# Kernel optimization log

Hardware: AMD Instinct MI355X
Metric: run time of the kernel (lower is better)

The kernel has to match this reference:

```python
import jax, jax.numpy as jnp
import numpy as np

N = 8192
IN = 128   # in_channels
CH = 64    # conv_ch


def setup_inputs() -> dict:
    key = jax.random.key(0)
    ks = jax.random.split(key, 8)
    p = lambda k, shape: jax.random.normal(k, shape, jnp.float32) * 0.02
    return {
        "x": jax.random.normal(ks[0], (N, IN), jnp.float32),
        "edge_index": jax.random.randint(ks[1], (N, N), 0, 2, jnp.int32),
        "W1": p(ks[2], (IN, CH)),      "b1": jnp.zeros((CH,), jnp.float32),
        "W2": p(ks[3], (CH, 2 * CH)),  "b2": jnp.zeros((2 * CH,), jnp.float32),
        "We": p(ks[4], (2 * CH, CH)),  "be": jnp.zeros((CH,), jnp.float32),
        "Wd1": p(ks[5], (2 * CH, CH)), "bd1": jnp.zeros((CH,), jnp.float32),
        "Wd2": p(ks[6], (CH, IN)),     "bd2": jnp.zeros((IN,), jnp.float32),
    }


def _norm_adj(edge_index):
    # PyG GCNConv: A_hat = A + I (self loops appended), sym norm D^-1/2 A_hat D^-1/2
    A = (edge_index != 0).astype(jnp.float32)
    A = A + jnp.eye(A.shape[0], dtype=jnp.float32)
    deg = A.sum(axis=1)
    dinv = jnp.where(deg > 0.0, jax.lax.rsqrt(deg), 0.0)
    return dinv[:, None] * A * dinv[None, :]  # [N, N]


def _gcn(nadj, x, W, b):
    return nadj @ (x @ W) + b


def _lrelu(v):
    return jax.nn.leaky_relu(v, 0.01)  # torch default negative_slope


def reference(x, edge_index, W1, b1, W2, b2, We, be, Wd1, bd1, Wd2, bd2):
    nadj = _norm_adj(edge_index)
    h = _lrelu(_gcn(nadj, x, W1, b1))          # [N, CH]
    z = _lrelu(_gcn(nadj, h, W2, b2))          # [N, 2*CH]
    re = _lrelu(_gcn(nadj, z, We, be))         # [N, CH]
    recon_edge = jax.nn.sigmoid(re @ re.T)     # [N, N]
    xd = _lrelu(_gcn(nadj, z, Wd1, bd1))       # [N, CH]
    x_out = _lrelu(_gcn(nadj, xd, Wd2, bd2))   # [N, IN]
    return (recon_edge, x_out, z)
```

## Files before the change

### kernel.cpp

```cpp
#include <hip/hip_runtime.h>
#include <hip/hip_bf16.h>
#include <stdint.h>

typedef unsigned short u16;
typedef unsigned char u8;
typedef unsigned int u32;
typedef __attribute__((ext_vector_type(8))) short frag8;
typedef __attribute__((ext_vector_type(4))) float f4;

#define N8K 8192
#define SK 4
#define NKT 256
#define NT2 128


__device__ __forceinline__ u16 f2bf(float f) {
  union { float f; unsigned u; } v; v.f = f;
  return (u16)((v.u + 0x7FFFu + ((v.u >> 16) & 1u)) >> 16);
}
__device__ __forceinline__ float lrelu(float v) { return v > 0.f ? v : 0.01f * v; }

__device__ __forceinline__ void expand4(u32 w, u32& o0, u32& o1) {
  u32 hi = __builtin_amdgcn_perm(0u, 0x00403F00u, w);
  u32 lo = __builtin_amdgcn_perm(0u, 0x00008000u, w);
  o0 = __builtin_amdgcn_perm(hi, lo, 0x05010400u);
  o1 = __builtin_amdgcn_perm(hi, lo, 0x07030602u);
}

#define WQ(col) (((col) & 31) >> 3)
#define SHIFT(col) (8 * (((col) & 7) & 3) + 2 * (((col) & 7) >> 2) + 4 * ((col) >> 5))

__global__ __launch_bounds__(256) void k_deg(const int* __restrict__ e,
                                             u8* __restrict__ at,
                                             float* __restrict__ dinv) {
  int Rt = blockIdx.x;
  int t = threadIdx.x;
  int rl = t & 15;
  int row = Rt * 16 + rl;
  int tg = t >> 4;
  int diagT2 = row >> 6;
  int cnt = 0;
  __shared__ int cs[256];
  for (int p = 0; p < 8; ++p) {
    int T2 = tg + 16 * p;
    const int4* src = (const int4*)(e + (size_t)row * N8K + T2 * 64);
    u32 w[4] = {0u, 0u, 0u, 0u};
#pragma unroll
    for (int q8 = 0; q8 < 16; ++q8) {
      int4 v = src[q8];
      u32 c0 = (v.x != 0), c1 = (v.y != 0), c2 = (v.z != 0), c3 = (v.w != 0);
      cnt += (int)(c0 + c1 + c2 + c3);
      const int cb = q8 * 4;
      w[WQ(cb + 0)] |= c0 << SHIFT(cb + 0);
      w[WQ(cb + 1)] |= c1 << SHIFT(cb + 1);
      w[WQ(cb + 2)] |= c2 << SHIFT(cb + 2);
      w[WQ(cb + 3)] |= c3 << SHIFT(cb + 3);
    }
    if (T2 == diagT2) {
      int col = row & 63;
      int qd = (col & 31) >> 3;
      u32 add = 1u << (8 * ((col & 7) & 3) + 2 * ((col & 7) >> 2) + 4 * (col >> 5));
#pragma unroll
      for (int q = 0; q < 4; ++q)
        if (q == qd) w[q] += add;
      cnt += 1;
    }
    u8* dst = at + ((size_t)(Rt * NT2 + T2) * 64 + rl) * 4;
#pragma unroll
    for (int q = 0; q < 4; ++q)
      *(u32*)(dst + (size_t)(16 * q) * 4) = w[q];
  }
  cs[t] = cnt;
  __syncthreads();
  if (t < 16) {
    int s = 0;
#pragma unroll
    for (int g = 0; g < 16; ++g) s += cs[t + 16 * g];
    dinv[Rt * 16 + t] = 1.0f / sqrtf((float)s);
  }
}

__global__ __launch_bounds__(256, 2) void k_sgemm1(const float* __restrict__ Xf,
                                                   const float* __restrict__ Wa,
                                                   const float* __restrict__ dinv,
                                                   u16* __restrict__ Pt) {
  const int KT = 4;
  __shared__ __attribute__((aligned(16))) u16 Wt[8 * 4 * 64 * 8];
  int t = threadIdx.x, mt = blockIdx.x;
  int lane = t & 63, wave = t >> 6;
  for (int u = t; u < 8 * KT * 64; u += 256) {
    int l = u & 63, T = (u >> 6) % KT, nt = (u >> 6) / KT;
    int n = nt * 16 + (l & 15);
    int k0 = T * 32 + (l >> 4) * 8;
    u16 tmp[8];
#pragma unroll
    for (int j = 0; j < 8; ++j) {
      int k = k0 + j;
      float v = (n < 64) ? Wa[k * 64 + n] : 0.f;
      tmp[j] = f2bf(v);
    }
    *(uint4*)&Wt[(size_t)u * 8] = *(const uint4*)tmp;
  }
  __syncthreads();
  int wm = (wave >> 1) * 64, wn = (wave & 1) * 64;
  int fm = lane & 15, q = lane >> 4;
  f4 acc[4][4];
#pragma unroll
  for (int m = 0; m < 4; ++m)
#pragma unroll
    for (int n = 0; n < 4; ++n) acc[m][n] = (f4){0.f, 0.f, 0.f, 0.f};
  for (int T = 0; T < KT; ++T) {
    frag8 a[4], b[4];
#pragma unroll
    for (int m = 0; m < 4; ++m) {
      int Rt = mt * 8 + (wm >> 4) + m;
      const float* px = Xf + (size_t)(Rt * 16 + fm) * 128 + T * 32 + q * 8;
      float4 v0 = *(const float4*)px, v1 = *(const float4*)(px + 4);
      u16 tmp[8] = {f2bf(v0.x), f2bf(v0.y), f2bf(v0.z), f2bf(v0.w),
                    f2bf(v1.x), f2bf(v1.y), f2bf(v1.z), f2bf(v1.w)};
      a[m] = *(const frag8*)tmp;
    }
#pragma unroll
    for (int n = 0; n < 4; ++n)
      b[n] = *(const frag8*)&Wt[((size_t)(((wn >> 4) + n) * KT + T) * 64 + lane) * 8];
#pragma unroll
    for (int m = 0; m < 4; ++m)
#pragma unroll
      for (int n = 0; n < 4; ++n)
        acc[m][n] = __builtin_amdgcn_mfma_f32_16x16x32_bf16(a[m], b[n], acc[m][n], 0, 0, 0);
  }
#pragma unroll
  for (int m = 0; m < 4; ++m) {
    int ibase = mt * 128 + wm + 16 * m + q * 4;
    float d0 = dinv[ibase], d1 = dinv[ibase + 1], d2 = dinv[ibase + 2], d3 = dinv[ibase + 3];
#pragma unroll
    for (int n = 0; n < 4; ++n) {
      u32 lo = (u32)f2bf(d0 * acc[m][n][0]) | ((u32)f2bf(d1 * acc[m][n][1]) << 16);
      u32 hi = (u32)f2bf(d2 * acc[m][n][2]) | ((u32)f2bf(d3 * acc[m][n][3]) << 16);
      u32 plo = __shfl_xor(lo, 16, 64);
      u32 phi = __shfl_xor(hi, 16, 64);
      if ((q & 1) == 0) {
        uint4 u; u.x = lo; u.y = hi; u.z = plo; u.w = phi;
        int gi = mt * 128 + wm + 16 * m + (q >> 1) * 8;
        int T2 = gi >> 5;
        int lB = fm + 16 * ((gi >> 3) & 3);
        int nt = (wn >> 4) + n;
        *(uint4*)(Pt + ((size_t)(nt * NKT + T2) * 64 + lB) * 8) = u;
      }
    }
  }
}

__global__ __launch_bounds__(256, 1) void k_bgemm(const u8* __restrict__ At,
                                                  const u16* __restrict__ Bt,
                                                  float* __restrict__ Ctmp) {
  int t = threadIdx.x;
  int mt = blockIdx.x, ks = blockIdx.y;
  int lane = t & 63, wave = t >> 6;
  int wm = (wave >> 1) * 64, wn = (wave & 1) * 64;
  f4 acc[4][4];
#pragma unroll
  for (int m = 0; m < 4; ++m)
#pragma unroll
    for (int n = 0; n < 4; ++n) acc[m][n] = (f4){0.f, 0.f, 0.f, 0.f};

  const int T20 = ks * 32;
  const u8*  Ab = At + ((size_t)((mt * 8 + (wm >> 4)) * NT2 + T20) * 64 + lane) * 4;
  const u16* Bb = Bt + ((size_t)(((wn >> 4)) * NKT + 2 * T20) * 64 + lane) * 8;

#pragma unroll 2
  for (int T2 = 0; T2 < 32; ++T2) {
    u32 w[4];
    frag8 aE[4], aO[4], bE[4], bO[4];
#pragma unroll
    for (int m = 0; m < 4; ++m)
      w[m] = *(const u32*)(Ab + (size_t)m * (NT2 * 256) + (size_t)T2 * 256);
#pragma unroll
    for (int n = 0; n < 4; ++n) {
      bE[n] = *(const frag8*)(Bb + (size_t)n * (NKT * 512) + (size_t)(2 * T2) * 512);
      bO[n] = *(const frag8*)(Bb + (size_t)n * (NKT * 512) + (size_t)(2 * T2) * 512 + 512);
    }
#pragma unroll
    for (int m = 0; m < 4; ++m) {
      u32 e0 = w[m] & 0x03030303u;
      u32 e1 = (w[m] >> 2) & 0x03030303u;
      u32 e2 = (w[m] >> 4) & 0x03030303u;
      u32 e3 = (w[m] >> 6) & 0x03030303u;
      uint4 rE, rO;
      expand4(e0, rE.x, rE.y); expand4(e1, rE.z, rE.w);
      expand4(e2, rO.x, rO.y); expand4(e3, rO.z, rO.w);
      aE[m] = *(const frag8*)&rE;
      aO[m] = *(const frag8*)&rO;
    }
#pragma unroll
    for (int m = 0; m < 4; ++m)
#pragma unroll
      for (int n = 0; n < 4; ++n)
        acc[m][n] = __builtin_amdgcn_mfma_f32_16x16x32_bf16(aE[m], bE[n], acc[m][n], 0, 0, 0);
#pragma unroll
    for (int m = 0; m < 4; ++m)
#pragma unroll
      for (int n = 0; n < 4; ++n)
        acc[m][n] = __builtin_amdgcn_mfma_f32_16x16x32_bf16(aO[m], bO[n], acc[m][n], 0, 0, 0);
  }

  float* Co = Ctmp + (size_t)ks * (N8K * 128);
  int fm = lane & 15, rbase = (lane >> 4) * 4;
#pragma unroll
  for (int m = 0; m < 4; ++m) {
    int i0 = mt * 128 + wm + 16 * m + rbase;
#pragma unroll
    for (int n = 0; n < 4; ++n) {
      int c = wn + 16 * n + fm;
#pragma unroll
      for (int r = 0; r < 4; ++r) Co[(size_t)(i0 + r) * 128 + c] = acc[m][n][r];
    }
  }
}

__global__ __launch_bounds__(256, 2) void k_fuse(const float* __restrict__ Ctmp,
                                                 const float* __restrict__ dinv,
                                                 const float* __restrict__ bE,
                                                 const float* __restrict__ bE2,
                                                 float* __restrict__ outZ,
                                                 u16* __restrict__ retG,
                                                 int mode,
                                                 const float* __restrict__ Wa, int wacols,
                                                 const float* __restrict__ Wb,
                                                 u16* __restrict__ Pt) {
  __shared__ __attribute__((aligned(16))) u16 Xs[8 * 4 * 64 * 8];
  __shared__ __attribute__((aligned(16))) u16 Wt[8 * 4 * 64 * 8];
  int t = threadIdx.x, mt = blockIdx.x;
  int lane = t & 63, wave = t >> 6;
  const int KT = (mode == 2) ? 4 : 2;

  int C8 = (mode == 1) ? 8 : 16;
  int totalU = 128 * C8;
  for (int u0 = t; u0 < totalU; u0 += 256) {
    int i = (mode == 1) ? (u0 >> 3) : (u0 >> 4);
    int c8 = (mode == 1) ? (u0 & 7) : (u0 & 15);
    int gi = mt * 128 + i;
    int c0 = c8 * 8;
    float v[8];
#pragma unroll
    for (int j = 0; j < 8; ++j) v[j] = 0.f;
#pragma unroll
    for (int k = 0; k < SK; ++k) {
      const float4* p = (const float4*)(Ctmp + (size_t)k * (N8K * 128) + (size_t)gi * 128 + c0);
      float4 x0 = p[0], x1 = p[1];
      v[0] += x0.x; v[1] += x0.y; v[2] += x0.z; v[3] += x0.w;
      v[4] += x1.x; v[5] += x1.y; v[6] += x1.z; v[7] += x1.w;
    }
    float di = dinv[gi];
    u16 ob[8];
    if (mode == 3 && c8 < 8) {
#pragma unroll
      for (int j = 0; j < 8; ++j) ob[j] = f2bf(lrelu(di * v[j] + bE[c0 + j]));
      int T = c8 >> 2, l = (i & 15) + 16 * (c8 & 3);
      *(uint4*)(retG + ((size_t)((gi >> 4) * 2 + T) * 64 + l) * 8) = *(const uint4*)ob;
    } else if (mode == 3) {
      int cl = c0 - 64;
#pragma unroll
      for (int j = 0; j < 8; ++j) ob[j] = f2bf(lrelu(di * v[j] + bE2[cl + j]));
      int cp = c8 - 8;
      int T = cp >> 2, l = (i & 15) + 16 * (cp & 3);
      *(uint4*)&Xs[(((i >> 4) * 2 + T) * 64 + l) * 8] = *(const uint4*)ob;
    } else {
#pragma unroll
      for (int j = 0; j < 8; ++j) v[j] = lrelu(di * v[j] + bE[c0 + j]);
#pragma unroll
      for (int j = 0; j < 8; ++j) ob[j] = f2bf(v[j]);
      int T = c8 >> 2, l = (i & 15) + 16 * (c8 & 3);
      *(uint4*)&Xs[(((i >> 4) * KT + T) * 64 + l) * 8] = *(const uint4*)ob;
      if (mode == 2) {
        float4* po = (float4*)(outZ + (size_t)gi * 128 + c0);
        po[0] = (float4){v[0], v[1], v[2], v[3]};
        po[1] = (float4){v[4], v[5], v[6], v[7]};
      }
    }
  }

  for (int u = t; u < 8 * KT * 64; u += 256) {
    int l = u & 63, T = (u >> 6) % KT, nt = (u >> 6) / KT;
    int n = nt * 16 + (l & 15);
    int k0 = T * 32 + (l >> 4) * 8;
    u16 tmp[8];
#pragma unroll
    for (int j = 0; j < 8; ++j) {
      int k = k0 + j;
      float v = (n < wacols) ? Wa[k * wacols + n] : (Wb ? Wb[k * 64 + (n - 64)] : 0.f);
      tmp[j] = f2bf(v);
    }
    *(uint4*)&Wt[(size_t)u * 8] = *(const uint4*)tmp;
  }
  __syncthreads();

  int wm = (wave >> 1) * 64, wn = (wave & 1) * 64;
  int fm = lane & 15, q = lane >> 4;
  f4 acc[4][4];
#pragma unroll
  for (int m = 0; m < 4; ++m)
#pragma unroll
    for (int n = 0; n < 4; ++n) acc[m][n] = (f4){0.f, 0.f, 0.f, 0.f};
  for (int T = 0; T < KT; ++T) {
    frag8 a[4], b[4];
#pragma unroll
    for (int m = 0; m < 4; ++m)
      a[m] = *(const frag8*)&Xs[((size_t)(((wm >> 4) + m) * KT + T) * 64 + lane) * 8];
#pragma unroll
    for (int n = 0; n < 4; ++n)
      b[n] = *(const frag8*)&Wt[((size_t)(((wn >> 4) + n) * KT + T) * 64 + lane) * 8];
#pragma unroll
    for (int m = 0; m < 4; ++m)
#pragma unroll
      for (int n = 0; n < 4; ++n)
        acc[m][n] = __builtin_amdgcn_mfma_f32_16x16x32_bf16(a[m], b[n], acc[m][n], 0, 0, 0);
  }
#pragma unroll
  for (int m = 0; m < 4; ++m) {
    int ibase = mt * 128 + wm + 16 * m + q * 4;
    float d0 = dinv[ibase], d1 = dinv[ibase + 1], d2 = dinv[ibase + 2], d3 = dinv[ibase + 3];
#pragma unroll
    for (int n = 0; n < 4; ++n) {
      u32 lo = (u32)f2bf(d0 * acc[m][n][0]) | ((u32)f2bf(d1 * acc[m][n][1]) << 16);
      u32 hi = (u32)f2bf(d2 * acc[m][n][2]) | ((u32)f2bf(d3 * acc[m][n][3]) << 16);
      u32 plo = __shfl_xor(lo, 16, 64);
      u32 phi = __shfl_xor(hi, 16, 64);
      if ((q & 1) == 0) {
        uint4 u; u.x = lo; u.y = hi; u.z = plo; u.w = phi;
        int gi = mt * 128 + wm + 16 * m + (q >> 1) * 8;
        int T2 = gi >> 5;
        int lB = fm + 16 * ((gi >> 3) & 3);
        int nt = (wn >> 4) + n;
        *(uint4*)(Pt + ((size_t)(nt * NKT + T2) * 64 + lB) * 8) = u;
      }
    }
  }
}

__global__ __launch_bounds__(256) void k_epi4(const float* __restrict__ Ctmp,
                                              const float* __restrict__ dinv,
                                              const float* __restrict__ bA,
                                              float* __restrict__ outF) {
  int idx = blockIdx.x * 256 + threadIdx.x;
  int i = idx >> 4, c8 = idx & 15;
  int c0 = c8 * 8;
  float v[8];
#pragma unroll
  for (int j = 0; j < 8; ++j) v[j] = 0.f;
#pragma unroll
  for (int k = 0; k < SK; ++k) {
    const float4* p = (const float4*)(Ctmp + (size_t)k * (N8K * 128) + (size_t)i * 128 + c0);
    float4 x0 = p[0], x1 = p[1];
    v[0] += x0.x; v[1] += x0.y; v[2] += x0.z; v[3] += x0.w;
    v[4] += x1.x; v[5] += x1.y; v[6] += x1.z; v[7] += x1.w;
  }
  float di = dinv[i];
#pragma unroll
  for (int j = 0; j < 8; ++j) v[j] = lrelu(di * v[j] + bA[c0 + j]);
  float4* po = (float4*)(outF + (size_t)i * 128 + c0);
  po[0] = (float4){v[0], v[1], v[2], v[3]};
  po[1] = (float4){v[4], v[5], v[6], v[7]};
}

__global__ __launch_bounds__(256, 4) void k_recon(const u16* __restrict__ ret,
                                                  float* __restrict__ out) {
  int t = threadIdx.x;
  int bi = blockIdx.x, bj = blockIdx.y;
  int lane = t & 63, wave = t >> 6;
  int wm = (wave >> 1) * 64, wn = (wave & 1) * 64;
  int fm = lane & 15;
  f4 acc[4][4];
#pragma unroll
  for (int m = 0; m < 4; ++m)
#pragma unroll
    for (int n = 0; n < 4; ++n) acc[m][n] = (f4){0.f, 0.f, 0.f, 0.f};
#pragma unroll
  for (int T = 0; T < 2; ++T) {
    frag8 a[4], b[4];
#pragma unroll
    for (int m = 0; m < 4; ++m)
      a[m] = *(const frag8*)(ret + ((size_t)((bi * 8 + (wm >> 4) + m) * 2 + T) * 64 + lane) * 8);
#pragma unroll
    for (int n = 0; n < 4; ++n)
      b[n] = *(const frag8*)(ret + ((size_t)((bj * 8 + (wn >> 4) + n) * 2 + T) * 64 + lane) * 8);
#pragma unroll
    for (int m = 0; m < 4; ++m)
#pragma unroll
      for (int n = 0; n < 4; ++n)
        acc[m][n] = __builtin_amdgcn_mfma_f32_16x16x32_bf16(a[m], b[n], acc[m][n], 0, 0, 0);
  }
  int rbase = (lane >> 4) * 4;
#pragma unroll
  for (int m = 0; m < 4; ++m) {
#pragma unroll
    for (int n = 0; n < 4; ++n) {
      int gj = bj * 128 + wn + 16 * n + fm;
#pragma unroll
      for (int r = 0; r < 4; ++r) {
        int gi = bi * 128 + wm + 16 * m + rbase + r;
        float ex = __builtin_amdgcn_exp2f(acc[m][n][r] * -1.442695041f);
        out[(size_t)gi * N8K + gj] = __builtin_amdgcn_rcpf(1.0f + ex);
      }
    }
  }
}

extern "C" void kernel_launch(void* const* d_in, const int* in_sizes, int n_in,
                              void* d_out, int out_size, void* d_ws, size_t ws_size,
                              hipStream_t stream) {
  const float* x   = (const float*)d_in[0];
  const int*   e   = (const int*)d_in[1];
  const float* W1  = (const float*)d_in[2];
  const float* b1  = (const float*)d_in[3];
  const float* W2  = (const float*)d_in[4];
  const float* b2  = (const float*)d_in[5];
  const float* We  = (const float*)d_in[6];
  const float* be  = (const float*)d_in[7];
  const float* Wd1 = (const float*)d_in[8];
  const float* bd1 = (const float*)d_in[9];
  const float* Wd2 = (const float*)d_in[10];
  const float* bd2 = (const float*)d_in[11];

  float* out       = (float*)d_out;
  float* out_recon = out;
  float* out_x     = out + 67108864;
  float* out_z     = out + 67108864 + 1048576;

  u8*    at   = (u8*)d_out;
  float* Ctmp = out + 16777216;

  char* ws = (char*)d_ws;
  float* dinv = (float*)(ws);
  u16* Pt  = (u16*)(ws + 32768);
  u16* ret = (u16*)(ws + 32768 + 2097152);

  k_deg<<<512, 256, 0, stream>>>(e, at, dinv);

  k_sgemm1<<<64, 256, 0, stream>>>(x, W1, dinv, Pt);
  k_bgemm<<<dim3(64, SK), 256, 0, stream>>>(at, Pt, Ctmp);

  k_fuse<<<64, 256, 0, stream>>>(Ctmp, dinv, b1, nullptr, nullptr, nullptr, 1,
                                 W2, 128, nullptr, Pt);
  k_bgemm<<<dim3(64, SK), 256, 0, stream>>>(at, Pt, Ctmp);

  k_fuse<<<64, 256, 0, stream>>>(Ctmp, dinv, b2, nullptr, out_z, nullptr, 2,
                                 We, 64, Wd1, Pt);
  k_bgemm<<<dim3(64, SK), 256, 0, stream>>>(at, Pt, Ctmp);

  k_fuse<<<64, 256, 0, stream>>>(Ctmp, dinv, be, bd1, nullptr, ret, 3,
                                 Wd2, 128, nullptr, Pt);
  k_bgemm<<<dim3(64, SK), 256, 0, stream>>>(at, Pt, Ctmp);

  k_epi4<<<512, 256, 0, stream>>>(Ctmp, dinv, bd2, out_x);

  k_recon<<<dim3(64, 64), 256, 0, stream>>>(ret, out_recon);
}
```

Baseline: 655.4 us.

## Shrink GEMM tiles to raise block count and skip padded columns in first layer

The adjacency GEMM now uses 64-row blocks (128x4 grid instead of 64x4), with a templated variant that computes only 64 real output columns for the first layer instead of padding to 128. The fused epilogue and small GEMMs use 32-row and 64-row tiles so more blocks fill the GPU's compute units. Occupancy is raised to 2 blocks per CU. In exchange, each block reuses its B fragments over fewer rows, so B operand traffic per useful MFMA increases.

```diff
diff --git a/kernel.cpp b/kernel.cpp
--- a/kernel.cpp
+++ b/kernel.cpp
@@ -85,95 +85,80 @@
                                                    const float* __restrict__ dinv,
                                                    u16* __restrict__ Pt) {
   const int KT = 4;
-  __shared__ __attribute__((aligned(16))) u16 Wt[8 * 4 * 64 * 8];
+  __shared__ __attribute__((aligned(16))) u16 Wt[4 * 4 * 64 * 8];
   int t = threadIdx.x, mt = blockIdx.x;
   int lane = t & 63, wave = t >> 6;
-  for (int u = t; u < 8 * KT * 64; u += 256) {
+  for (int u = t; u < 4 * KT * 64; u += 256) {
     int l = u & 63, T = (u >> 6) % KT, nt = (u >> 6) / KT;
     int n = nt * 16 + (l & 15);
     int k0 = T * 32 + (l >> 4) * 8;
     u16 tmp[8];
 #pragma unroll
-    for (int j = 0; j < 8; ++j) {
-      int k = k0 + j;
-      float v = (n < 64) ? Wa[k * 64 + n] : 0.f;
-      tmp[j] = f2bf(v);
-    }
+    for (int j = 0; j < 8; ++j) tmp[j] = f2bf(Wa[(k0 + j) * 64 + n]);
     *(uint4*)&Wt[(size_t)u * 8] = *(const uint4*)tmp;
   }
   __syncthreads();
-  int wm = (wave >> 1) * 64, wn = (wave & 1) * 64;
   int fm = lane & 15, q = lane >> 4;
-  f4 acc[4][4];
-#pragma unroll
-  for (int m = 0; m < 4; ++m)
-#pragma unroll
-    for (int n = 0; n < 4; ++n) acc[m][n] = (f4){0.f, 0.f, 0.f, 0.f};
+  int Rt = mt * 4 + wave;
+  f4 acc[4];
+#pragma unroll
+  for (int n = 0; n < 4; ++n) acc[n] = (f4){0.f, 0.f, 0.f, 0.f};
   for (int T = 0; T < KT; ++T) {
-    frag8 a[4], b[4];
-#pragma unroll
-    for (int m = 0; m < 4; ++m) {
-      int Rt = mt * 8 + (wm >> 4) + m;
-      const float* px = Xf + (size_t)(Rt * 16 + fm) * 128 + T * 32 + q * 8;
-      float4 v0 = *(const float4*)px, v1 = *(const float4*)(px + 4);
-      u16 tmp[8] = {f2bf(v0.x), f2bf(v0.y), f2bf(v0.z), f2bf(v0.w),
-                    f2bf(v1.x), f2bf(v1.y), f2bf(v1.z), f2bf(v1.w)};
-      a[m] = *(const frag8*)tmp;
-    }
-#pragma unroll
-    for (int n = 0; n < 4; ++n)
-      b[n] = *(const frag8*)&Wt[((size_t)(((wn >> 4) + n) * KT + T) * 64 + lane) * 8];
-#pragma unroll
-    for (int m = 0; m < 4; ++m)
-#pragma unroll
-      for (int n = 0; n < 4; ++n)
-        acc[m][n] = __builtin_amdgcn_mfma_f32_16x16x32_bf16(a[m], b[n], acc[m][n], 0, 0, 0);
-  }
-#pragma unroll
-  for (int m = 0; m < 4; ++m) {
-    int ibase = mt * 128 + wm + 16 * m + q * 4;
-    float d0 = dinv[ibase], d1 = dinv[ibase + 1], d2 = dinv[ibase + 2], d3 = dinv[ibase + 3];
+    const float* px = Xf + (size_t)(Rt * 16 + fm) * 128 + T * 32 + q * 8;
+    float4 v0 = *(const float4*)px, v1 = *(const float4*)(px + 4);
+    u16 tmp[8] = {f2bf(v0.x), f2bf(v0.y), f2bf(v0.z), f2bf(v0.w),
+                  f2bf(v1.x), f2bf(v1.y), f2bf(v1.z), f2bf(v1.w)};
+    frag8 a = *(const frag8*)tmp;
 #pragma unroll
     for (int n = 0; n < 4; ++n) {
-      u32 lo = (u32)f2bf(d0 * acc[m][n][0]) | ((u32)f2bf(d1 * acc[m][n][1]) << 16);
-      u32 hi = (u32)f2bf(d2 * acc[m][n][2]) | ((u32)f2bf(d3 * acc[m][n][3]) << 16);
-      u32 plo = __shfl_xor(lo, 16, 64);
-      u32 phi = __shfl_xor(hi, 16, 64);
-      if ((q & 1) == 0) {
-        uint4 u; u.x = lo; u.y = hi; u.z = plo; u.w = phi;
-        int gi = mt * 128 + wm + 16 * m + (q >> 1) * 8;
-        int T2 = gi >> 5;
-        int lB = fm + 16 * ((gi >> 3) & 3);
-        int nt = (wn >> 4) + n;
-        *(uint4*)(Pt + ((size_t)(nt * NKT + T2) * 64 + lB) * 8) = u;
-      }
-    }
-  }
-}
-
-__global__ __launch_bounds__(256, 1) void k_bgemm(const u8* __restrict__ At,
+      frag8 b = *(const frag8*)&Wt[((size_t)(n * KT + T) * 64 + lane) * 8];
+      acc[n] = __builtin_amdgcn_mfma_f32_16x16x32_bf16(a, b, acc[n], 0, 0, 0);
+    }
+  }
+  int ibase = Rt * 16 + q * 4;
+  float d0 = dinv[ibase], d1 = dinv[ibase + 1], d2 = dinv[ibase + 2], d3 = dinv[ibase + 3];
+#pragma unroll
+  for (int n = 0; n < 4; ++n) {
+    u32 lo = (u32)f2bf(d0 * acc[n][0]) | ((u32)f2bf(d1 * acc[n][1]) << 16);
+    u32 hi = (u32)f2bf(d2 * acc[n][2]) | ((u32)f2bf(d3 * acc[n][3]) << 16);
+    u32 plo = __shfl_xor(lo, 16, 64);
+    u32 phi = __shfl_xor(hi, 16, 64);
+    if ((q & 1) == 0) {
+      uint4 u; u.x = lo; u.y = hi; u.z = plo; u.w = phi;
+      int gi = Rt * 16 + (q >> 1) * 8;
+      int T2 = gi >> 5;
+      int lB = fm + 16 * ((gi >> 3) & 3);
+      *(uint4*)(Pt + ((size_t)(n * NKT + T2) * 64 + lB) * 8) = u;
+    }
+  }
+}
+
+template<int NCT>
+__global__ __launch_bounds__(256, 2) void k_bgemm(const u8* __restrict__ At,
                                                   const u16* __restrict__ Bt,
                                                   float* __restrict__ Ctmp) {
   int t = threadIdx.x;
   int mt = blockIdx.x, ks = blockIdx.y;
   int lane = t & 63, wave = t >> 6;
-  int wm = (wave >> 1) * 64, wn = (wave & 1) * 64;
-  f4 acc[4][4];
-#pragma unroll
-  for (int m = 0; m < 4; ++m)
+  constexpr int WR = (NCT == 8) ? 2 : 1;
+  const int rtb = (NCT == 8) ? (mt * 4 + (wave >> 1) * 2) : (mt * 4 + wave);
+  const int ctb = (NCT == 8) ? ((wave & 1) * 4) : 0;
+  f4 acc[WR][4];
+#pragma unroll
+  for (int m = 0; m < WR; ++m)
 #pragma unroll
     for (int n = 0; n < 4; ++n) acc[m][n] = (f4){0.f, 0.f, 0.f, 0.f};
 
   const int T20 = ks * 32;
-  const u8*  Ab = At + ((size_t)((mt * 8 + (wm >> 4)) * NT2 + T20) * 64 + lane) * 4;
-  const u16* Bb = Bt + ((size_t)(((wn >> 4)) * NKT + 2 * T20) * 64 + lane) * 8;
+  const u8*  Ab = At + ((size_t)(rtb * NT2 + T20) * 64 + lane) * 4;
+  const u16* Bb = Bt + ((size_t)(ctb * NKT + 2 * T20) * 64 + lane) * 8;
 
 #pragma unroll 2
   for (int T2 = 0; T2 < 32; ++T2) {
-    u32 w[4];
-    frag8 aE[4], aO[4], bE[4], bO[4];
-#pragma unroll
-    for (int m = 0; m < 4; ++m)
+    u32 w[WR];
+    frag8 aE[WR], aO[WR], bE[4], bO[4];
+#pragma unroll
+    for (int m = 0; m < WR; ++m)
       w[m] = *(const u32*)(Ab + (size_t)m * (NT2 * 256) + (size_t)T2 * 256);
 #pragma unroll
     for (int n = 0; n < 4; ++n) {
@@ -181,7 +166,7 @@
       bO[n] = *(const frag8*)(Bb + (size_t)n * (NKT * 512) + (size_t)(2 * T2) * 512 + 512);
     }
 #pragma unroll
-    for (int m = 0; m < 4; ++m) {
+    for (int m = 0; m < WR; ++m) {
       u32 e0 = w[m] & 0x03030303u;
       u32 e1 = (w[m] >> 2) & 0x03030303u;
       u32 e2 = (w[m] >> 4) & 0x03030303u;
@@ -193,27 +178,28 @@
       aO[m] = *(const frag8*)&rO;
     }
 #pragma unroll
-    for (int m = 0; m < 4; ++m)
+    for (int m = 0; m < WR; ++m)
 #pragma unroll
       for (int n = 0; n < 4; ++n)
         acc[m][n] = __builtin_amdgcn_mfma_f32_16x16x32_bf16(aE[m], bE[n], acc[m][n], 0, 0, 0);
 #pragma unroll
-    for (int m = 0; m < 4; ++m)
+    for (int m = 0; m < WR; ++m)
 #pragma unroll
       for (int n = 0; n < 4; ++n)
         acc[m][n] = __builtin_amdgcn_mfma_f32_16x16x32_bf16(aO[m], bO[n], acc[m][n], 0, 0, 0);
   }
 
-  float* Co = Ctmp + (size_t)ks * (N8K * 128);
+  constexpr int CST = NCT * 16;
+  float* Co = Ctmp + (size_t)ks * (N8K * CST);
   int fm = lane & 15, rbase = (lane >> 4) * 4;
 #pragma unroll
-  for (int m = 0; m < 4; ++m) {
-    int i0 = mt * 128 + wm + 16 * m + rbase;
+  for (int m = 0; m < WR; ++m) {
+    int i0 = mt * 64 + ((NCT == 8) ? ((wave >> 1) * 32) : (wave * 16)) + 16 * m + rbase;
 #pragma unroll
     for (int n = 0; n < 4; ++n) {
-      int c = wn + 16 * n + fm;
-#pragma unroll
-      for (int r = 0; r < 4; ++r) Co[(size_t)(i0 + r) * 128 + c] = acc[m][n][r];
+      int c = ctb * 16 + 16 * n + fm;
+#pragma unroll
+      for (int r = 0; r < 4; ++r) Co[(size_t)(i0 + r) * CST + c] = acc[m][n][r];
     }
   }
 }
@@ -228,25 +214,26 @@
                                                  const float* __restrict__ Wa, int wacols,
                                                  const float* __restrict__ Wb,
                                                  u16* __restrict__ Pt) {
-  __shared__ __attribute__((aligned(16))) u16 Xs[8 * 4 * 64 * 8];
+  __shared__ __attribute__((aligned(16))) u16 Xs[2 * 4 * 64 * 8];
   __shared__ __attribute__((aligned(16))) u16 Wt[8 * 4 * 64 * 8];
   int t = threadIdx.x, mt = blockIdx.x;
   int lane = t & 63, wave = t >> 6;
   const int KT = (mode == 2) ? 4 : 2;
+  const int cst = (mode == 1) ? 64 : 128;
 
   int C8 = (mode == 1) ? 8 : 16;
-  int totalU = 128 * C8;
+  int totalU = 32 * C8;
   for (int u0 = t; u0 < totalU; u0 += 256) {
     int i = (mode == 1) ? (u0 >> 3) : (u0 >> 4);
     int c8 = (mode == 1) ? (u0 & 7) : (u0 & 15);
-    int gi = mt * 128 + i;
+    int gi = mt * 32 + i;
     int c0 = c8 * 8;
     float v[8];
 #pragma unroll
     for (int j = 0; j < 8; ++j) v[j] = 0.f;
 #pragma unroll
     for (int k = 0; k < SK; ++k) {
-      const float4* p = (const float4*)(Ctmp + (size_t)k * (N8K * 128) + (size_t)gi * 128 + c0);
+      const float4* p = (const float4*)(Ctmp + (size_t)k * (N8K * cst) + (size_t)gi * cst + c0);
       float4 x0 = p[0], x1 = p[1];
       v[0] += x0.x; v[1] += x0.y; v[2] += x0.z; v[3] += x0.w;
       v[4] += x1.x; v[5] += x1.y; v[6] += x1.z; v[7] += x1.w;
@@ -264,7 +251,7 @@
       for (int j = 0; j < 8; ++j) ob[j] = f2bf(lrelu(di * v[j] + bE2[cl + j]));
       int cp = c8 - 8;
       int T = cp >> 2, l = (i & 15) + 16 * (cp & 3);
-      *(uint4*)&Xs[(((i >> 4) * 2 + T) * 64 + l) * 8] = *(const uint4*)ob;
+      *(uint4*)&Xs[(((i >> 4) * KT + T) * 64 + l) * 8] = *(const uint4*)ob;
     } else {
 #pragma unroll
       for (int j = 0; j < 8; ++j) v[j] = lrelu(di * v[j] + bE[c0 + j]);
@@ -295,45 +282,35 @@
   }
   __syncthreads();
 
-  int wm = (wave >> 1) * 64, wn = (wave & 1) * 64;
   int fm = lane & 15, q = lane >> 4;
-  f4 acc[4][4];
-#pragma unroll
-  for (int m = 0; m < 4; ++m)
-#pragma unroll
-    for (int n = 0; n < 4; ++n) acc[m][n] = (f4){0.f, 0.f, 0.f, 0.f};
+  int rt = wave >> 1;
+  int cb = (wave & 1) * 4;
+  f4 acc[4];
+#pragma unroll
+  for (int n = 0; n < 4; ++n) acc[n] = (f4){0.f, 0.f, 0.f, 0.f};
   for (int T = 0; T < KT; ++T) {
-    frag8 a[4], b[4];
-#pragma unroll
-    for (int m = 0; m < 4; ++m)
-      a[m] = *(const frag8*)&Xs[((size_t)(((wm >> 4) + m) * KT + T) * 64 + lane) * 8];
-#pragma unroll
-    for (int n = 0; n < 4; ++n)
-      b[n] = *(const frag8*)&Wt[((size_t)(((wn >> 4) + n) * KT + T) * 64 + lane) * 8];
-#pragma unroll
-    for (int m = 0; m < 4; ++m)
-#pragma unroll
-      for (int n = 0; n < 4; ++n)
-        acc[m][n] = __builtin_amdgcn_mfma_f32_16x16x32_bf16(a[m], b[n], acc[m][n], 0, 0, 0);
-  }
-#pragma unroll
-  for (int m = 0; m < 4; ++m) {
-    int ibase = mt * 128 + wm + 16 * m + q * 4;
-    float d0 = dinv[ibase], d1 = dinv[ibase + 1], d2 = dinv[ibase + 2], d3 = dinv[ibase + 3];
+    frag8 a = *(const frag8*)&Xs[((size_t)(rt * KT + T) * 64 + lane) * 8];
 #pragma unroll
     for (int n = 0; n < 4; ++n) {
-      u32 lo = (u32)f2bf(d0 * acc[m][n][0]) | ((u32)f2bf(d1 * acc[m][n][1]) << 16);
-      u32 hi = (u32)f2bf(d2 * acc[m][n][2]) | ((u32)f2bf(d3 * acc[m][n][3]) << 16);
-      u32 plo = __shfl_xor(lo, 16, 64);
-      u32 phi = __shfl_xor(hi, 16, 64);
-      if ((q & 1) == 0) {
-        uint4 u; u.x = lo; u.y = hi; u.z = plo; u.w = phi;
-        int gi = mt * 128 + wm + 16 * m + (q >> 1) * 8;
-        int T2 = gi >> 5;
-        int lB = fm + 16 * ((gi >> 3) & 3);
-        int nt = (wn >> 4) + n;
-        *(uint4*)(Pt + ((size_t)(nt * NKT + T2) * 64 + lB) * 8) = u;
-      }
+      frag8 b = *(const frag8*)&Wt[((size_t)((cb + n) * KT + T) * 64 + lane) * 8];
+      acc[n] = __builtin_amdgcn_mfma_f32_16x16x32_bf16(a, b, acc[n], 0, 0, 0);
+    }
+  }
+  int ibase = mt * 32 + rt * 16 + q * 4;
+  float d0 = dinv[ibase], d1 = dinv[ibase + 1], d2 = dinv[ibase + 2], d3 = dinv[ibase + 3];
+#pragma unroll
+  for (int n = 0; n < 4; ++n) {
+    u32 lo = (u32)f2bf(d0 * acc[n][0]) | ((u32)f2bf(d1 * acc[n][1]) << 16);
+    u32 hi = (u32)f2bf(d2 * acc[n][2]) | ((u32)f2bf(d3 * acc[n][3]) << 16);
+    u32 plo = __shfl_xor(lo, 16, 64);
+    u32 phi = __shfl_xor(hi, 16, 64);
+    if ((q & 1) == 0) {
+      uint4 u; u.x = lo; u.y = hi; u.z = plo; u.w = phi;
+      int gi = mt * 32 + rt * 16 + (q >> 1) * 8;
+      int T2 = gi >> 5;
+      int lB = fm + 16 * ((gi >> 3) & 3);
+      int nt = cb + n;
+      *(uint4*)(Pt + ((size_t)(nt * NKT + T2) * 64 + lB) * 8) = u;
     }
   }
 }
@@ -437,20 +414,20 @@
 
   k_deg<<<512, 256, 0, stream>>>(e, at, dinv);
 
-  k_sgemm1<<<64, 256, 0, stream>>>(x, W1, dinv, Pt);
-  k_bgemm<<<dim3(64, SK), 256, 0, stream>>>(at, Pt, Ctmp);
-
-  k_fuse<<<64, 256, 0, stream>>>(Ctmp, dinv, b1, nullptr, nullptr, nullptr, 1,
-                                 W2, 128, nullptr, Pt);
-  k_bgemm<<<dim3(64, SK), 256, 0, stream>>>(at, Pt, Ctmp);
-
-  k_fuse<<<64, 256, 0, stream>>>(Ctmp, dinv, b2, nullptr, out_z, nullptr, 2,
-                                 We, 64, Wd1, Pt);
-  k_bgemm<<<dim3(64, SK), 256, 0, stream>>>(at, Pt, Ctmp);
-
-  k_fuse<<<64, 256, 0, stream>>>(Ctmp, dinv, be, bd1, nullptr, ret, 3,
-                                 Wd2, 128, nullptr, Pt);
-  k_bgemm<<<dim3(64, SK), 256, 0, stream>>>(at, Pt, Ctmp);
+  k_sgemm1<<<128, 256, 0, stream>>>(x, W1, dinv, Pt);
+  k_bgemm<4><<<dim3(128, SK), 256, 0, stream>>>(at, Pt, Ctmp);
+
+  k_fuse<<<256, 256, 0, stream>>>(Ctmp, dinv, b1, nullptr, nullptr, nullptr, 1,
+                                  W2, 128, nullptr, Pt);
+  k_bgemm<8><<<dim3(128, SK), 256, 0, stream>>>(at, Pt, Ctmp);
+
+  k_fuse<<<256, 256, 0, stream>>>(Ctmp, dinv, b2, nullptr, out_z, nullptr, 2,
+                                  We, 64, Wd1, Pt);
+  k_bgemm<8><<<dim3(128, SK), 256, 0, stream>>>(at, Pt, Ctmp);
+
+  k_fuse<<<256, 256, 0, stream>>>(Ctmp, dinv, be, bd1, nullptr, ret, 3,
+                                  Wd2, 128, nullptr, Pt);
+  k_bgemm<8><<<dim3(128, SK), 256, 0, stream>>>(at, Pt, Ctmp);
 
   k_epi4<<<512, 256, 0, stream>>>(Ctmp, dinv, bd2, out_x);
 
```

Measured after the change: 645.0 us. About the same (-1.6%).
